# Kernel tuning notes

Measured on AMD Instinct MI355X. Metric: run time of the kernel, lower is better.

Reference implementation:

```python
import jax, jax.numpy as jnp
import numpy as np

NUM_GRAPHS = 1024
IN_F = 256
HID = 512


def setup_inputs() -> dict:
    key = jax.random.key(0)
    ks = jax.random.split(key, 20)
    s_in = 1.0 / np.sqrt(IN_F)
    s_h = 1.0 / np.sqrt(HID)
    inp = {
        "x": jax.random.normal(ks[0], (200000, IN_F), dtype=jnp.float32),
        "batch": jnp.sort(jax.random.randint(ks[1], (200000,), 0, NUM_GRAPHS)),
        # transforms: Linear(in_features -> hidden)
        "W_mean": jax.random.uniform(ks[2], (IN_F, HID), jnp.float32, -s_in, s_in),
        "b_mean": jax.random.uniform(ks[3], (HID,), jnp.float32, -s_in, s_in),
        "W_max": jax.random.uniform(ks[4], (IN_F, HID), jnp.float32, -s_in, s_in),
        "b_max": jax.random.uniform(ks[5], (HID,), jnp.float32, -s_in, s_in),
        "W_sum": jax.random.uniform(ks[6], (IN_F, HID), jnp.float32, -s_in, s_in),
        "b_sum": jax.random.uniform(ks[7], (HID,), jnp.float32, -s_in, s_in),
        # gates: Linear(hidden -> 1) + sigmoid
        "g_mean_w": jax.random.uniform(ks[8], (HID, 1), jnp.float32, -s_h, s_h),
        "g_mean_b": jax.random.uniform(ks[9], (1,), jnp.float32, -s_h, s_h),
        "g_max_w": jax.random.uniform(ks[10], (HID, 1), jnp.float32, -s_h, s_h),
        "g_max_b": jax.random.uniform(ks[11], (1,), jnp.float32, -s_h, s_h),
        "g_sum_w": jax.random.uniform(ks[12], (HID, 1), jnp.float32, -s_h, s_h),
        "g_sum_b": jax.random.uniform(ks[13], (1,), jnp.float32, -s_h, s_h),
        # output proj: Linear(hidden -> in_features)
        "W_out": jax.random.uniform(ks[14], (HID, IN_F), jnp.float32, -s_h, s_h),
        "b_out": jax.random.uniform(ks[15], (IN_F,), jnp.float32, -s_h, s_h),
        # layer norm params
        "ln_gamma": jnp.ones((IN_F,), jnp.float32),
        "ln_beta": jnp.zeros((IN_F,), jnp.float32),
    }
    return inp


def reference(x, batch, W_mean, b_mean, W_max, b_max, W_sum, b_sum,
              g_mean_w, g_mean_b, g_max_w, g_max_b, g_sum_w, g_sum_b,
              W_out, b_out, ln_gamma, ln_beta):
    # --- segment pools over node dim ---
    sum_pool = jax.ops.segment_sum(x, batch, num_segments=NUM_GRAPHS)  # [G, F]
    counts = jax.ops.segment_sum(jnp.ones((x.shape[0],), x.dtype), batch,
                                 num_segments=NUM_GRAPHS)  # [G]
    mean_pool = sum_pool / jnp.maximum(counts, 1.0)[:, None]
    max_pool = jax.ops.segment_max(x, batch, num_segments=NUM_GRAPHS)
    max_pool = jnp.where(counts[:, None] > 0, max_pool, 0.0)

    # --- per-pool linear transforms ---
    mean_repr = mean_pool @ W_mean + b_mean  # [G, H]
    max_repr = max_pool @ W_max + b_max
    sum_repr = sum_pool @ W_sum + b_sum

    # --- gated fusion ---
    g_mean = jax.nn.sigmoid(mean_repr @ g_mean_w + g_mean_b)  # [G, 1]
    g_max = jax.nn.sigmoid(max_repr @ g_max_w + g_max_b)
    g_sum = jax.nn.sigmoid(sum_repr @ g_sum_w + g_sum_b)
    gates = jax.nn.softmax(jnp.concatenate([g_mean, g_max, g_sum], axis=1), axis=1)
    pooled = (gates[:, 0:1] * mean_repr + gates[:, 1:2] * max_repr
              + gates[:, 2:3] * sum_repr)

    # --- output projection (+dropout as eval identity) + layer norm ---
    emb = pooled @ W_out + b_out  # [G, F]
    mu = jnp.mean(emb, axis=-1, keepdims=True)
    var = jnp.var(emb, axis=-1, keepdims=True)
    emb = (emb - mu) * jax.lax.rsqrt(var + 1e-5) * ln_gamma + ln_beta
    return emb
```

## Files before the change

### kernel.cpp

```cpp
#include <hip/hip_runtime.h>
#include <math.h>

#define NUM_GRAPHS 1024
#define IN_F 256
#define HID 512

__device__ __forceinline__ int lower_bound_i(const int* __restrict__ b, int n, int v) {
    int lo = 0, hi = n;
    while (lo < hi) {
        int mid = (lo + hi) >> 1;
        if (b[mid] < v) lo = mid + 1; else hi = mid;
    }
    return lo;
}

__global__ __launch_bounds__(256) void pool_kernel(
    const float* __restrict__ x, const int* __restrict__ batch, int N,
    float* __restrict__ sum_pool, float* __restrict__ mean_pool,
    float* __restrict__ max_pool)
{
    int g = blockIdx.x;
    __shared__ int sb[2];
    if (threadIdx.x < 2) sb[threadIdx.x] = lower_bound_i(batch, N, g + (int)threadIdx.x);
    __syncthreads();
    int start = sb[0], end = sb[1];
    int cnt = end - start;
    int w = threadIdx.x >> 6, lane = threadIdx.x & 63;
    const float4* x4 = (const float4*)x;
    float4 s = make_float4(0.f, 0.f, 0.f, 0.f);
    float4 m = make_float4(-INFINITY, -INFINITY, -INFINITY, -INFINITY);
    int r = start + w;
    for (; r + 12 < end; r += 16) {
        float4 v0 = x4[(size_t)(r     )*64 + lane];
        float4 v1 = x4[(size_t)(r +  4)*64 + lane];
        float4 v2 = x4[(size_t)(r +  8)*64 + lane];
        float4 v3 = x4[(size_t)(r + 12)*64 + lane];
        s.x += (v0.x+v1.x)+(v2.x+v3.x); s.y += (v0.y+v1.y)+(v2.y+v3.y);
        s.z += (v0.z+v1.z)+(v2.z+v3.z); s.w += (v0.w+v1.w)+(v2.w+v3.w);
        m.x = fmaxf(m.x, fmaxf(fmaxf(v0.x,v1.x), fmaxf(v2.x,v3.x)));
        m.y = fmaxf(m.y, fmaxf(fmaxf(v0.y,v1.y), fmaxf(v2.y,v3.y)));
        m.z = fmaxf(m.z, fmaxf(fmaxf(v0.z,v1.z), fmaxf(v2.z,v3.z)));
        m.w = fmaxf(m.w, fmaxf(fmaxf(v0.w,v1.w), fmaxf(v2.w,v3.w)));
    }
    for (; r < end; r += 4) {
        float4 v = x4[(size_t)r*64 + lane];
        s.x += v.x; s.y += v.y; s.z += v.z; s.w += v.w;
        m.x = fmaxf(m.x, v.x); m.y = fmaxf(m.y, v.y);
        m.z = fmaxf(m.z, v.z); m.w = fmaxf(m.w, v.w);
    }
    __shared__ float4 Ls[4][64];
    __shared__ float4 Lm[4][64];
    Ls[w][lane] = s; Lm[w][lane] = m;
    __syncthreads();
    if (w == 0) {
        float4 s0 = Ls[0][lane], s1 = Ls[1][lane], s2 = Ls[2][lane], s3 = Ls[3][lane];
        float4 m0 = Lm[0][lane], m1 = Lm[1][lane], m2 = Lm[2][lane], m3 = Lm[3][lane];
        float4 st, mt;
        st.x = (s0.x+s1.x)+(s2.x+s3.x); st.y = (s0.y+s1.y)+(s2.y+s3.y);
        st.z = (s0.z+s1.z)+(s2.z+s3.z); st.w = (s0.w+s1.w)+(s2.w+s3.w);
        mt.x = fmaxf(fmaxf(m0.x,m1.x), fmaxf(m2.x,m3.x));
        mt.y = fmaxf(fmaxf(m0.y,m1.y), fmaxf(m2.y,m3.y));
        mt.z = fmaxf(fmaxf(m0.z,m1.z), fmaxf(m2.z,m3.z));
        mt.w = fmaxf(fmaxf(m0.w,m1.w), fmaxf(m2.w,m3.w));
        float inv = 1.0f / fmaxf((float)cnt, 1.0f);
        float4 me = make_float4(st.x*inv, st.y*inv, st.z*inv, st.w*inv);
        if (cnt == 0) mt = make_float4(0.f, 0.f, 0.f, 0.f);
        size_t o = (size_t)g*64 + lane;
        ((float4*)sum_pool)[o]  = st;
        ((float4*)mean_pool)[o] = me;
        ((float4*)max_pool)[o]  = mt;
    }
}

#define BM 64
#define BN 64
#define BK 16
#define LDA 68
__global__ __launch_bounds__(256) void transform_gemm(
    const float* __restrict__ p_mean, const float* __restrict__ p_max, const float* __restrict__ p_sum,
    const float* __restrict__ Wm, const float* __restrict__ bm_,
    const float* __restrict__ Wx, const float* __restrict__ bx_,
    const float* __restrict__ Wsm, const float* __restrict__ bs_,
    float* __restrict__ r_mean, float* __restrict__ r_max, float* __restrict__ r_sum)
{
    int z = blockIdx.z;
    const float* P    = (z==0) ? p_mean : (z==1) ? p_max : p_sum;
    const float* W    = (z==0) ? Wm     : (z==1) ? Wx    : Wsm;
    const float* bias = (z==0) ? bm_    : (z==1) ? bx_   : bs_;
    float* R          = (z==0) ? r_mean : (z==1) ? r_max : r_sum;

    __shared__ float As[BK][LDA];
    __shared__ float Bs[BK][LDA];
    int tid = threadIdx.x;
    int bm0 = blockIdx.y * BM;
    int bn0 = blockIdx.x * BN;
    int tx = tid & 15, ty = tid >> 4;
    int arow = tid >> 2, akq = (tid & 3) * 4;
    int brow = tid >> 4, bn4 = (tid & 15) * 4;
    float acc[4][4] = {};

    for (int kc = 0; kc < IN_F; kc += BK) {
        float4 av = *(const float4*)&P[(size_t)(bm0 + arow)*IN_F + kc + akq];
        float4 bv = *(const float4*)&W[(size_t)(kc + brow)*HID + bn0 + bn4];
        As[akq+0][arow] = av.x; As[akq+1][arow] = av.y;
        As[akq+2][arow] = av.z; As[akq+3][arow] = av.w;
        *(float4*)&Bs[brow][bn4] = bv;
        __syncthreads();
        #pragma unroll
        for (int k = 0; k < BK; ++k) {
            float4 a = *(const float4*)&As[k][ty*4];
            float4 b = *(const float4*)&Bs[k][tx*4];
            acc[0][0] += a.x*b.x; acc[0][1] += a.x*b.y; acc[0][2] += a.x*b.z; acc[0][3] += a.x*b.w;
            acc[1][0] += a.y*b.x; acc[1][1] += a.y*b.y; acc[1][2] += a.y*b.z; acc[1][3] += a.y*b.w;
            acc[2][0] += a.z*b.x; acc[2][1] += a.z*b.y; acc[2][2] += a.z*b.z; acc[2][3] += a.z*b.w;
            acc[3][0] += a.w*b.x; acc[3][1] += a.w*b.y; acc[3][2] += a.w*b.z; acc[3][3] += a.w*b.w;
        }
        __syncthreads();
    }
    float4 b4 = *(const float4*)&bias[bn0 + tx*4];
    #pragma unroll
    for (int i = 0; i < 4; ++i) {
        float4 o = make_float4(acc[i][0]+b4.x, acc[i][1]+b4.y, acc[i][2]+b4.z, acc[i][3]+b4.w);
        *(float4*)&R[(size_t)(bm0 + ty*4 + i)*HID + bn0 + tx*4] = o;
    }
}

#define EM 4
__global__ __launch_bounds__(256) void gate_outproj_ln(
    const float* __restrict__ r_mean, const float* __restrict__ r_max, const float* __restrict__ r_sum,
    const float* __restrict__ gwm, const float* __restrict__ gbm,
    const float* __restrict__ gwx, const float* __restrict__ gbx,
    const float* __restrict__ gws, const float* __restrict__ gbs,
    const float* __restrict__ Wout, const float* __restrict__ bout,
    const float* __restrict__ gamma, const float* __restrict__ beta,
    float* __restrict__ out)
{
    int g0 = blockIdx.x * EM;
    int tid = threadIdx.x;
    __shared__ float Rm[EM][HID], Rx[EM][HID], Rs[EM][HID];
    __shared__ float Ps[EM][HID];
    __shared__ float Es[EM][IN_F];
    __shared__ float wgt[EM][3];

    const float4* rm4 = (const float4*)(r_mean + (size_t)g0*HID);
    const float4* rx4 = (const float4*)(r_max  + (size_t)g0*HID);
    const float4* rs4 = (const float4*)(r_sum  + (size_t)g0*HID);
    #pragma unroll
    for (int i = 0; i < 2; ++i) {
        int idx = tid + i*256;
        ((float4*)Rm)[idx] = rm4[idx];
        ((float4*)Rx)[idx] = rx4[idx];
        ((float4*)Rs)[idx] = rs4[idx];
    }
    __syncthreads();

    int w = tid >> 6, lane = tid & 63;
    float dm = 0.f, dx = 0.f, dsv = 0.f;
    #pragma unroll
    for (int j = 0; j < 8; ++j) {
        int k = lane + j*64;
        dm  += Rm[w][k] * gwm[k];
        dx  += Rx[w][k] * gwx[k];
        dsv += Rs[w][k] * gws[k];
    }
    #pragma unroll
    for (int off = 32; off > 0; off >>= 1) {
        dm  += __shfl_xor(dm,  off, 64);
        dx  += __shfl_xor(dx,  off, 64);
        dsv += __shfl_xor(dsv, off, 64);
    }
    if (lane == 0) {
        float sm = 1.f/(1.f + expf(-(dm  + gbm[0])));
        float sx = 1.f/(1.f + expf(-(dx  + gbx[0])));
        float ss = 1.f/(1.f + expf(-(dsv + gbs[0])));
        float em = expf(sm), ex = expf(sx), es = expf(ss);
        float inv = 1.f/(em + ex + es);
        wgt[w][0] = em*inv; wgt[w][1] = ex*inv; wgt[w][2] = es*inv;
    }
    __syncthreads();

    #pragma unroll
    for (int i = 0; i < 8; ++i) {
        int e = tid + i*256;
        int j = e >> 9, k = e & 511;
        Ps[j][k] = wgt[j][0]*Rm[j][k] + wgt[j][1]*Rx[j][k] + wgt[j][2]*Rs[j][k];
    }
    __syncthreads();

    float a0 = 0.f, a1 = 0.f, a2 = 0.f, a3 = 0.f;
    int f = tid;
    for (int k = 0; k < HID; k += 4) {
        float4 p0 = *(const float4*)&Ps[0][k];
        float4 p1 = *(const float4*)&Ps[1][k];
        float4 p2 = *(const float4*)&Ps[2][k];
        float4 p3 = *(const float4*)&Ps[3][k];
        float w0 = Wout[(size_t)(k+0)*IN_F + f];
        float w1 = Wout[(size_t)(k+1)*IN_F + f];
        float w2 = Wout[(size_t)(k+2)*IN_F + f];
        float w3 = Wout[(size_t)(k+3)*IN_F + f];
        a0 += p0.x*w0 + p0.y*w1 + p0.z*w2 + p0.w*w3;
        a1 += p1.x*w0 + p1.y*w1 + p1.z*w2 + p1.w*w3;
        a2 += p2.x*w0 + p2.y*w1 + p2.z*w2 + p2.w*w3;
        a3 += p3.x*w0 + p3.y*w1 + p3.z*w2 + p3.w*w3;
    }
    float bo = bout[f];
    Es[0][f] = a0 + bo; Es[1][f] = a1 + bo; Es[2][f] = a2 + bo; Es[3][f] = a3 + bo;
    __syncthreads();

    float v0 = Es[w][lane], v1 = Es[w][lane+64], v2 = Es[w][lane+128], v3 = Es[w][lane+192];
    float s  = (v0+v1) + (v2+v3);
    float sq = (v0*v0 + v1*v1) + (v2*v2 + v3*v3);
    #pragma unroll
    for (int off = 32; off > 0; off >>= 1) {
        s  += __shfl_xor(s,  off, 64);
        sq += __shfl_xor(sq, off, 64);
    }
    float mu  = s * (1.0f/IN_F);
    float var = sq * (1.0f/IN_F) - mu*mu;
    float rs  = rsqrtf(var + 1e-5f);
    float* orow = out + (size_t)(g0 + w)*IN_F;
    orow[lane]     = (v0-mu)*rs*gamma[lane]     + beta[lane];
    orow[lane+64]  = (v1-mu)*rs*gamma[lane+64]  + beta[lane+64];
    orow[lane+128] = (v2-mu)*rs*gamma[lane+128] + beta[lane+128];
    orow[lane+192] = (v3-mu)*rs*gamma[lane+192] + beta[lane+192];
}

extern "C" void kernel_launch(void* const* d_in, const int* in_sizes, int n_in,
                              void* d_out, int out_size, void* d_ws, size_t ws_size,
                              hipStream_t stream)
{
    const float* x        = (const float*)d_in[0];
    const int*   batch    = (const int*)d_in[1];
    const float* W_mean   = (const float*)d_in[2];
    const float* b_mean   = (const float*)d_in[3];
    const float* W_max    = (const float*)d_in[4];
    const float* b_max    = (const float*)d_in[5];
    const float* W_sum    = (const float*)d_in[6];
    const float* b_sum    = (const float*)d_in[7];
    const float* g_mean_w = (const float*)d_in[8];
    const float* g_mean_b = (const float*)d_in[9];
    const float* g_max_w  = (const float*)d_in[10];
    const float* g_max_b  = (const float*)d_in[11];
    const float* g_sum_w  = (const float*)d_in[12];
    const float* g_sum_b  = (const float*)d_in[13];
    const float* W_out    = (const float*)d_in[14];
    const float* b_out    = (const float*)d_in[15];
    const float* ln_gamma = (const float*)d_in[16];
    const float* ln_beta  = (const float*)d_in[17];
    float* out = (float*)d_out;
    int N = in_sizes[1];

    float* ws        = (float*)d_ws;
    float* sum_pool  = ws;
    float* mean_pool = ws + (size_t)NUM_GRAPHS*IN_F;
    float* max_pool  = ws + (size_t)2*NUM_GRAPHS*IN_F;
    float* r_mean    = ws + (size_t)3*NUM_GRAPHS*IN_F;
    float* r_max     = r_mean + (size_t)NUM_GRAPHS*HID;
    float* r_sum     = r_max  + (size_t)NUM_GRAPHS*HID;

    pool_kernel<<<NUM_GRAPHS, 256, 0, stream>>>(x, batch, N, sum_pool, mean_pool, max_pool);

    dim3 gridC(HID/BN, NUM_GRAPHS/BM, 3);
    transform_gemm<<<gridC, 256, 0, stream>>>(mean_pool, max_pool, sum_pool,
                                              W_mean, b_mean, W_max, b_max, W_sum, b_sum,
                                              r_mean, r_max, r_sum);

    gate_outproj_ln<<<NUM_GRAPHS/EM, 256, 0, stream>>>(r_mean, r_max, r_sum,
                                                       g_mean_w, g_mean_b, g_max_w, g_max_b,
                                                       g_sum_w, g_sum_b,
                                                       W_out, b_out, ln_gamma, ln_beta, out);
}
```

Baseline: 404.5 us.

## Use bf16 MFMA for pool transforms and precompute segment boundaries

Replaces the fp32 SIMT tiled GEMM for the three pool transforms with bf16 MFMA 16x16x32 instructions. A new prep kernel transposes and converts the weights to bf16 on every call, and also builds segment offsets once instead of running a binary search per block. The pool kernel now writes bf16 pooled outputs. This cuts GEMM compute and per-block search latency, but adds an extra launch and bf16 rounding error, which is large on the unnormalized sum pool.

After: 394.3 us. -2.5%, faster.

```diff
diff --git a/kernel.cpp b/kernel.cpp
--- a/kernel.cpp
+++ b/kernel.cpp
@@ -5,25 +5,58 @@
 #define IN_F 256
 #define HID 512
 
-__device__ __forceinline__ int lower_bound_i(const int* __restrict__ b, int n, int v) {
-    int lo = 0, hi = n;
-    while (lo < hi) {
-        int mid = (lo + hi) >> 1;
-        if (b[mid] < v) lo = mid + 1; else hi = mid;
-    }
-    return lo;
+typedef __bf16 bf16x4 __attribute__((ext_vector_type(4)));
+typedef __bf16 bf16x8 __attribute__((ext_vector_type(8)));
+typedef float  f32x4  __attribute__((ext_vector_type(4)));
+
+__global__ __launch_bounds__(256) void prep_kernel(
+    const float* __restrict__ Wm, const float* __restrict__ Wx, const float* __restrict__ Wsm,
+    __bf16* __restrict__ wt,
+    const int* __restrict__ batch, int N, int* __restrict__ seg)
+{
+    int b = blockIdx.x;
+    if (b < 96) {
+        __shared__ float tile[64][65];
+        int z  = b / 32;
+        int kt = (b % 32) / 8, nt = b % 8;
+        const float* W = (z==0) ? Wm : (z==1) ? Wx : Wsm;
+        __bf16* Wt = wt + (size_t)z * HID * IN_F;
+        int k0 = kt * 64, n0 = nt * 64;
+        int r  = threadIdx.x >> 2;
+        int c0 = (threadIdx.x & 3) * 16;
+        #pragma unroll
+        for (int j = 0; j < 4; ++j) {
+            float4 v = *(const float4*)&W[(size_t)(k0 + r)*HID + n0 + c0 + j*4];
+            tile[r][c0+j*4+0] = v.x; tile[r][c0+j*4+1] = v.y;
+            tile[r][c0+j*4+2] = v.z; tile[r][c0+j*4+3] = v.w;
+        }
+        __syncthreads();
+        #pragma unroll
+        for (int j = 0; j < 4; ++j) {
+            bf16x4 o;
+            o.x = (__bf16)tile[c0+j*4+0][r];
+            o.y = (__bf16)tile[c0+j*4+1][r];
+            o.z = (__bf16)tile[c0+j*4+2][r];
+            o.w = (__bf16)tile[c0+j*4+3][r];
+            *(bf16x4*)&Wt[(size_t)(n0 + r)*IN_F + k0 + c0 + j*4] = o;
+        }
+    } else {
+        int i = (b - 96) * 256 + threadIdx.x;
+        if (i <= N) {
+            int cur  = (i < N) ? batch[i] : NUM_GRAPHS;
+            int prev = (i == 0) ? -1 : batch[i-1];
+            for (int g = prev + 1; g <= cur; ++g) seg[g] = i;
+        }
+    }
 }
 
 __global__ __launch_bounds__(256) void pool_kernel(
-    const float* __restrict__ x, const int* __restrict__ batch, int N,
-    float* __restrict__ sum_pool, float* __restrict__ mean_pool,
-    float* __restrict__ max_pool)
+    const float* __restrict__ x, const int* __restrict__ seg,
+    __bf16* __restrict__ pool_mean, __bf16* __restrict__ pool_max,
+    __bf16* __restrict__ pool_sum)
 {
     int g = blockIdx.x;
-    __shared__ int sb[2];
-    if (threadIdx.x < 2) sb[threadIdx.x] = lower_bound_i(batch, N, g + (int)threadIdx.x);
-    __syncthreads();
-    int start = sb[0], end = sb[1];
+    int start = seg[g], end = seg[g+1];
     int cnt = end - start;
     int w = threadIdx.x >> 6, lane = threadIdx.x & 63;
     const float4* x4 = (const float4*)x;
@@ -63,65 +96,62 @@
         mt.z = fmaxf(fmaxf(m0.z,m1.z), fmaxf(m2.z,m3.z));
         mt.w = fmaxf(fmaxf(m0.w,m1.w), fmaxf(m2.w,m3.w));
         float inv = 1.0f / fmaxf((float)cnt, 1.0f);
-        float4 me = make_float4(st.x*inv, st.y*inv, st.z*inv, st.w*inv);
         if (cnt == 0) mt = make_float4(0.f, 0.f, 0.f, 0.f);
+        bf16x4 sb, mb, xb;
+        sb.x = (__bf16)st.x;       sb.y = (__bf16)st.y;
+        sb.z = (__bf16)st.z;       sb.w = (__bf16)st.w;
+        mb.x = (__bf16)(st.x*inv); mb.y = (__bf16)(st.y*inv);
+        mb.z = (__bf16)(st.z*inv); mb.w = (__bf16)(st.w*inv);
+        xb.x = (__bf16)mt.x;       xb.y = (__bf16)mt.y;
+        xb.z = (__bf16)mt.z;       xb.w = (__bf16)mt.w;
         size_t o = (size_t)g*64 + lane;
-        ((float4*)sum_pool)[o]  = st;
-        ((float4*)mean_pool)[o] = me;
-        ((float4*)max_pool)[o]  = mt;
-    }
-}
-
-#define BM 64
-#define BN 64
-#define BK 16
-#define LDA 68
-__global__ __launch_bounds__(256) void transform_gemm(
-    const float* __restrict__ p_mean, const float* __restrict__ p_max, const float* __restrict__ p_sum,
-    const float* __restrict__ Wm, const float* __restrict__ bm_,
-    const float* __restrict__ Wx, const float* __restrict__ bx_,
-    const float* __restrict__ Wsm, const float* __restrict__ bs_,
+        ((bf16x4*)pool_sum)[o]  = sb;
+        ((bf16x4*)pool_mean)[o] = mb;
+        ((bf16x4*)pool_max)[o]  = xb;
+    }
+}
+
+__global__ __launch_bounds__(256) void transform_mfma(
+    const __bf16* __restrict__ pm, const __bf16* __restrict__ px, const __bf16* __restrict__ ps,
+    const __bf16* __restrict__ wtm, const __bf16* __restrict__ wtx, const __bf16* __restrict__ wts,
+    const float* __restrict__ bm_, const float* __restrict__ bx_, const float* __restrict__ bs_,
     float* __restrict__ r_mean, float* __restrict__ r_max, float* __restrict__ r_sum)
 {
     int z = blockIdx.z;
-    const float* P    = (z==0) ? p_mean : (z==1) ? p_max : p_sum;
-    const float* W    = (z==0) ? Wm     : (z==1) ? Wx    : Wsm;
-    const float* bias = (z==0) ? bm_    : (z==1) ? bx_   : bs_;
-    float* R          = (z==0) ? r_mean : (z==1) ? r_max : r_sum;
-
-    __shared__ float As[BK][LDA];
-    __shared__ float Bs[BK][LDA];
-    int tid = threadIdx.x;
-    int bm0 = blockIdx.y * BM;
-    int bn0 = blockIdx.x * BN;
-    int tx = tid & 15, ty = tid >> 4;
-    int arow = tid >> 2, akq = (tid & 3) * 4;
-    int brow = tid >> 4, bn4 = (tid & 15) * 4;
-    float acc[4][4] = {};
-
-    for (int kc = 0; kc < IN_F; kc += BK) {
-        float4 av = *(const float4*)&P[(size_t)(bm0 + arow)*IN_F + kc + akq];
-        float4 bv = *(const float4*)&W[(size_t)(kc + brow)*HID + bn0 + bn4];
-        As[akq+0][arow] = av.x; As[akq+1][arow] = av.y;
-        As[akq+2][arow] = av.z; As[akq+3][arow] = av.w;
-        *(float4*)&Bs[brow][bn4] = bv;
-        __syncthreads();
-        #pragma unroll
-        for (int k = 0; k < BK; ++k) {
-            float4 a = *(const float4*)&As[k][ty*4];
-            float4 b = *(const float4*)&Bs[k][tx*4];
-            acc[0][0] += a.x*b.x; acc[0][1] += a.x*b.y; acc[0][2] += a.x*b.z; acc[0][3] += a.x*b.w;
-            acc[1][0] += a.y*b.x; acc[1][1] += a.y*b.y; acc[1][2] += a.y*b.z; acc[1][3] += a.y*b.w;
-            acc[2][0] += a.z*b.x; acc[2][1] += a.z*b.y; acc[2][2] += a.z*b.z; acc[2][3] += a.z*b.w;
-            acc[3][0] += a.w*b.x; acc[3][1] += a.w*b.y; acc[3][2] += a.w*b.z; acc[3][3] += a.w*b.w;
-        }
-        __syncthreads();
-    }
-    float4 b4 = *(const float4*)&bias[bn0 + tx*4];
-    #pragma unroll
-    for (int i = 0; i < 4; ++i) {
-        float4 o = make_float4(acc[i][0]+b4.x, acc[i][1]+b4.y, acc[i][2]+b4.z, acc[i][3]+b4.w);
-        *(float4*)&R[(size_t)(bm0 + ty*4 + i)*HID + bn0 + tx*4] = o;
+    const __bf16* A  = (z==0) ? pm  : (z==1) ? px  : ps;
+    const __bf16* Bt = (z==0) ? wtm : (z==1) ? wtx : wts;
+    const float* bias= (z==0) ? bm_ : (z==1) ? bx_ : bs_;
+    float* R         = (z==0) ? r_mean : (z==1) ? r_max : r_sum;
+
+    int bn0 = blockIdx.x * 64;
+    int bm0 = blockIdx.y * 64;
+    int w = threadIdx.x >> 6, lane = threadIdx.x & 63;
+    int qm = lane >> 4, rm = lane & 15;
+    const bf16x8* Arow = (const bf16x8*)(A + (size_t)(bm0 + w*16 + rm)*IN_F);
+    const bf16x8* B0 = (const bf16x8*)(Bt + (size_t)(bn0 +  0 + rm)*IN_F);
+    const bf16x8* B1 = (const bf16x8*)(Bt + (size_t)(bn0 + 16 + rm)*IN_F);
+    const bf16x8* B2 = (const bf16x8*)(Bt + (size_t)(bn0 + 32 + rm)*IN_F);
+    const bf16x8* B3 = (const bf16x8*)(Bt + (size_t)(bn0 + 48 + rm)*IN_F);
+    f32x4 a0 = {0.f,0.f,0.f,0.f}, a1 = a0, a2 = a0, a3 = a0;
+    #pragma unroll
+    for (int j = 0; j < 8; ++j) {
+        int fi = j*4 + qm;
+        bf16x8 af = Arow[fi];
+        a0 = __builtin_amdgcn_mfma_f32_16x16x32_bf16(af, B0[fi], a0, 0, 0, 0);
+        a1 = __builtin_amdgcn_mfma_f32_16x16x32_bf16(af, B1[fi], a1, 0, 0, 0);
+        a2 = __builtin_amdgcn_mfma_f32_16x16x32_bf16(af, B2[fi], a2, 0, 0, 0);
+        a3 = __builtin_amdgcn_mfma_f32_16x16x32_bf16(af, B3[fi], a3, 0, 0, 0);
+    }
+    int row0 = bm0 + w*16 + qm*4;
+    float b0 = bias[bn0 +  0 + rm], b1 = bias[bn0 + 16 + rm];
+    float b2 = bias[bn0 + 32 + rm], b3 = bias[bn0 + 48 + rm];
+    #pragma unroll
+    for (int r = 0; r < 4; ++r) {
+        float* Rr = R + (size_t)(row0 + r)*HID;
+        Rr[bn0 +  0 + rm] = a0[r] + b0;
+        Rr[bn0 + 16 + rm] = a1[r] + b1;
+        Rr[bn0 + 32 + rm] = a2[r] + b2;
+        Rr[bn0 + 48 + rm] = a3[r] + b3;
     }
 }
 
@@ -250,19 +280,28 @@
     float* out = (float*)d_out;
     int N = in_sizes[1];
 
-    float* ws        = (float*)d_ws;
-    float* sum_pool  = ws;
-    float* mean_pool = ws + (size_t)NUM_GRAPHS*IN_F;
-    float* max_pool  = ws + (size_t)2*NUM_GRAPHS*IN_F;
-    float* r_mean    = ws + (size_t)3*NUM_GRAPHS*IN_F;
-    float* r_max     = r_mean + (size_t)NUM_GRAPHS*HID;
-    float* r_sum     = r_max  + (size_t)NUM_GRAPHS*HID;
-
-    pool_kernel<<<NUM_GRAPHS, 256, 0, stream>>>(x, batch, N, sum_pool, mean_pool, max_pool);
-
-    dim3 gridC(HID/BN, NUM_GRAPHS/BM, 3);
-    transform_gemm<<<gridC, 256, 0, stream>>>(mean_pool, max_pool, sum_pool,
-                                              W_mean, b_mean, W_max, b_max, W_sum, b_sum,
+    float* ws      = (float*)d_ws;
+    float* r_mean  = ws;
+    float* r_max   = r_mean + (size_t)NUM_GRAPHS*HID;
+    float* r_sum   = r_max  + (size_t)NUM_GRAPHS*HID;
+    __bf16* pool_bf = (__bf16*)(r_sum + (size_t)NUM_GRAPHS*HID);
+    __bf16* pm  = pool_bf;
+    __bf16* px  = pm + (size_t)NUM_GRAPHS*IN_F;
+    __bf16* psu = px + (size_t)NUM_GRAPHS*IN_F;
+    __bf16* wt  = psu + (size_t)NUM_GRAPHS*IN_F;
+    __bf16* wtm = wt;
+    __bf16* wtx = wtm + (size_t)HID*IN_F;
+    __bf16* wts = wtx + (size_t)HID*IN_F;
+    int* seg    = (int*)(wts + (size_t)HID*IN_F);
+
+    int bnd_blocks = (N + 1 + 255) / 256;
+    prep_kernel<<<96 + bnd_blocks, 256, 0, stream>>>(W_mean, W_max, W_sum, wt, batch, N, seg);
+
+    pool_kernel<<<NUM_GRAPHS, 256, 0, stream>>>(x, seg, pm, px, psu);
+
+    dim3 gridC(HID/64, NUM_GRAPHS/64, 3);
+    transform_mfma<<<gridC, 256, 0, stream>>>(pm, px, psu, wtm, wtx, wts,
+                                              b_mean, b_max, b_sum,
                                               r_mean, r_max, r_sum);
 
     gate_outproj_ln<<<NUM_GRAPHS/EM, 256, 0, stream>>>(r_mean, r_max, r_sum,
```
